# Optimization experiments

Hardware: AMD Instinct MI355X
Metric: run time of the kernel (lower is better)

The kernel has to match this reference:

```python
import jax, jax.numpy as jnp
import numpy as np

STOCH_LENGTH = 8  # default `length` in Stochify.forward


def setup_inputs() -> dict:
    key = jax.random.key(0)
    k1, k2 = jax.random.split(key)
    B, K, N = 4096, 2048, 2048
    x = jax.random.normal(k1, (B, K), dtype=jnp.float32)
    # weight init: normal(0, sqrt(2/(in+out))), shape [out, in]
    weight = jax.random.normal(k2, (N, K), dtype=jnp.float32) * np.sqrt(2.0 / (K + N))
    bias = jnp.zeros((N,), dtype=jnp.float32)
    return {"x": x, "weight": weight, "bias": bias}


def _to_stoch(key, v, length):
    """Bipolar stochastic bitstream encode: bit_l ~ Bernoulli((v+1)/2), shape [L, *v.shape]."""
    p = jnp.clip((v + 1.0) * 0.5, 0.0, 1.0)
    u = jax.random.uniform(key, (length,) + v.shape, dtype=v.dtype)
    return (u < p).astype(v.dtype)


def reference(x, weight, bias):
    # Stochify.forward: api = to_stoch(input, L); apw = to_stoch(weight.t(), L)
    # out = stoch.mm(api, apw, bipolar=True, output_stoch=False) + bias
    # Bipolar stochastic multiply is XNOR of bits; decoded product value per (i,j,k):
    #   2/L * sum_l XNOR(a,b) - 1.  Summed over k:
    #   out[i,j] = (2/L) * sum_{k,l} (2 a b - a - b + 1) - K
    # which reduces to per-slice matmuls plus row/col bit-count corrections
    # (avoids materializing the [B,K,N,L] XNOR tensor).
    L = STOCH_LENGTH
    K = x.shape[1]
    kA, kB = jax.random.split(jax.random.key(42))
    A = _to_stoch(kA, x, L)            # [L, B, K] bits in {0,1}
    Wb = _to_stoch(kB, weight.T, L)    # [L, K, N]
    S = jnp.einsum('lbk,lkn->bn', A, Wb)  # sum_{k,l} a*b
    sA = A.sum(axis=(0, 2))            # [B]  sum_{k,l} a
    sB = Wb.sum(axis=(0, 1))           # [N]  sum_{k,l} b
    xnor_count = 2.0 * S - sA[:, None] - sB[None, :] + K * L
    out = (2.0 / L) * xnor_count - K
    return out + bias[None, :]
```

## Files before the change

### kernel.cpp

```cpp
#include <hip/hip_runtime.h>
#include <stdint.h>


#define B_DIM 4096
#define K_DIM 2048
#define N_DIM 2048
#define WORDS 256

typedef unsigned long long u64;

__host__ __device__ static inline void tf2x32(uint32_t ks0, uint32_t ks1,
                                              uint32_t x0, uint32_t x1,
                                              uint32_t* o0, uint32_t* o1) {
  uint32_t ks2 = ks0 ^ ks1 ^ 0x1BD11BDAu;
  x0 += ks0; x1 += ks1;
#define TF_RND(r) { x0 += x1; x1 = (x1 << (r)) | (x1 >> (32 - (r))); x1 ^= x0; }
  TF_RND(13) TF_RND(15) TF_RND(26) TF_RND(6)
  x0 += ks1; x1 += ks2 + 1u;
  TF_RND(17) TF_RND(29) TF_RND(16) TF_RND(24)
  x0 += ks2; x1 += ks0 + 2u;
  TF_RND(13) TF_RND(15) TF_RND(26) TF_RND(6)
  x0 += ks0; x1 += ks1 + 3u;
  TF_RND(17) TF_RND(29) TF_RND(16) TF_RND(24)
  x0 += ks1; x1 += ks2 + 4u;
  TF_RND(13) TF_RND(15) TF_RND(26) TF_RND(6)
  x0 += ks2; x1 += ks0 + 5u;
  *o0 = x0; *o1 = x1;
#undef TF_RND
}

__global__ __launch_bounds__(256) void stoch_bits(const float* __restrict__ x,
                                                  const float* __restrict__ wgt,
                                                  u64* __restrict__ Ap,
                                                  u64* __restrict__ Wp,
                                                  uint32_t xk0, uint32_t xk1,
                                                  uint32_t wk0, uint32_t wk1) {
  const unsigned blk = blockIdx.x;
  const bool isW = blk >= (unsigned)B_DIM;
  const unsigned row = isW ? (blk - (unsigned)B_DIM) : blk;
  const float* src = (isW ? wgt : x) + (size_t)row * K_DIM;
  u64* dst = (isW ? Wp : Ap) + (size_t)row * WORDS;
  const uint32_t k0 = isW ? wk0 : xk0;
  const uint32_t k1 = isW ? wk1 : xk1;
  const unsigned lane = threadIdx.x & 63u;
  const unsigned wv = threadIdx.x >> 6;
#pragma unroll 1
  for (int i = 0; i < 8; ++i) {
    const unsigned kw = wv * 8u + (unsigned)i;
    const unsigned k = (kw << 6) + lane;
    const float v = src[k];
    const float p = fminf(fmaxf((v + 1.0f) * 0.5f, 0.0f), 1.0f);
    const float t = p * 8388608.0f;
    const uint32_t base = isW ? (k * 2048u + row) : (row * 2048u + k);
    u64 wbuf[8];
#pragma unroll
    for (int l = 0; l < 8; ++l) {
      uint32_t idx = base + (isW ? ((uint32_t)l << 22) : ((uint32_t)l << 23));
      uint32_t o0, o1;
      tf2x32(k0, k1, 0u, idx, &o0, &o1);
      uint32_t m = (o0 ^ o1) >> 9;
      wbuf[l] = __ballot((float)m < t);
    }
    if (lane == 0) {
#pragma unroll
      for (int l = 0; l < 8; ++l) dst[(l << 5) + kw] = wbuf[l];
    }
  }
}

__global__ __launch_bounds__(256, 4) void xnor_gemm(const u64* __restrict__ Ap,
                                                    const u64* __restrict__ Wp,
                                                    const float* __restrict__ bias,
                                                    float* __restrict__ out) {
  __shared__ u64 As[128][18];
  __shared__ u64 Ws[64][18];
  const int tid = threadIdx.x;
  const int brow = blockIdx.y << 7;
  const int bcol = blockIdx.x << 6;
  const int tx = tid & 15, ty = tid >> 4;
  uint32_t cnt[8][4] = {};
#pragma unroll 1
  for (int c = 0; c < 16; ++c) {
    if (c) __syncthreads();
#pragma unroll
    for (int i = 0; i < 4; ++i) {
      int q = tid + (i << 8);
      int r = q >> 3, c4 = q & 7;
      *(uint4*)&As[r][c4 << 1] =
          *(const uint4*)&Ap[(size_t)(brow + r) * WORDS + (c << 4) + (c4 << 1)];
    }
#pragma unroll
    for (int i = 0; i < 2; ++i) {
      int q = tid + (i << 8);
      int r = q >> 3, c4 = q & 7;
      *(uint4*)&Ws[r][c4 << 1] =
          *(const uint4*)&Wp[(size_t)(bcol + r) * WORDS + (c << 4) + (c4 << 1)];
    }
    __syncthreads();
#pragma unroll 2
    for (int wp = 0; wp < 8; ++wp) {
      uint4 av[8], bv[4];
#pragma unroll
      for (int i = 0; i < 8; ++i)
        av[i] = *(const uint4*)&As[ty + (i << 4)][wp << 1];
#pragma unroll
      for (int j = 0; j < 4; ++j)
        bv[j] = *(const uint4*)&Ws[tx + (j << 4)][wp << 1];
#pragma unroll
      for (int i = 0; i < 8; ++i)
#pragma unroll
        for (int j = 0; j < 4; ++j) {
          uint32_t t0 = av[i].x ^ bv[j].x;
          uint32_t t1 = av[i].y ^ bv[j].y;
          uint32_t t2 = av[i].z ^ bv[j].z;
          uint32_t t3 = av[i].w ^ bv[j].w;
          asm("v_bcnt_u32_b32 %0, %1, %0" : "+v"(cnt[i][j]) : "v"(t0));
          asm("v_bcnt_u32_b32 %0, %1, %0" : "+v"(cnt[i][j]) : "v"(t1));
          asm("v_bcnt_u32_b32 %0, %1, %0" : "+v"(cnt[i][j]) : "v"(t2));
          asm("v_bcnt_u32_b32 %0, %1, %0" : "+v"(cnt[i][j]) : "v"(t3));
        }
    }
  }
#pragma unroll
  for (int i = 0; i < 8; ++i) {
    int r = brow + ty + (i << 4);
#pragma unroll
    for (int j = 0; j < 4; ++j) {
      int n = bcol + tx + (j << 4);
      out[(size_t)r * N_DIM + n] = 2048.0f - 0.25f * (float)cnt[i][j] + bias[n];
    }
  }
}

extern "C" void kernel_launch(void* const* d_in, const int* in_sizes, int n_in,
                              void* d_out, int out_size, void* d_ws, size_t ws_size,
                              hipStream_t stream) {
  const float* x = (const float*)d_in[0];
  const float* wgt = (const float*)d_in[1];
  const float* bias = (const float*)d_in[2];
  float* out = (float*)d_out;

  u64* Ap = (u64*)d_ws;
  u64* Wp = Ap + (size_t)B_DIM * WORDS;

  uint32_t kA0, kA1, kB0, kB1;
  tf2x32(0u, 42u, 0u, 0u, &kA0, &kA1);
  tf2x32(0u, 42u, 0u, 1u, &kB0, &kB1);

  stoch_bits<<<B_DIM + N_DIM, 256, 0, stream>>>(x, wgt, Ap, Wp, kA0, kA1, kB0, kB1);
  dim3 grid(N_DIM / 64, B_DIM / 128);
  xnor_gemm<<<grid, 256, 0, stream>>>(Ap, Wp, bias, out);
  (void)in_sizes; (void)n_in; (void)out_size; (void)ws_size;
}
```

Measured before the change: 501.6 us.

## Replace bit-packed XNOR popcount GEMM with int8 MFMA GEMM over byte bitstreams

The encoder now writes each stochastic bit as one byte in a [row, L*K] layout and computes per-row bit counts. The XNOR-popcount kernel is replaced by an int8 MFMA GEMM (32x32x32) that loads tiles with global_load_lds and applies the row and column count corrections in the epilogue. The aim is to run the inner product on matrix cores instead of the VALU popcount path, at the cost of 8x more workspace and memory traffic. This path is taken only when the workspace is large enough, otherwise it falls back to the old kernels.

```diff
diff --git a/kernel.cpp b/kernel.cpp
--- a/kernel.cpp
+++ b/kernel.cpp
@@ -6,8 +6,11 @@
 #define K_DIM 2048
 #define N_DIM 2048
 #define WORDS 256
+#define KL 16384
 
 typedef unsigned long long u64;
+typedef int v4i __attribute__((ext_vector_type(4)));
+typedef int v16i __attribute__((ext_vector_type(16)));
 
 __host__ __device__ static inline void tf2x32(uint32_t ks0, uint32_t ks1,
                                               uint32_t x0, uint32_t x1,
@@ -29,6 +32,127 @@
 #undef TF_RND
 }
 
+
+__global__ __launch_bounds__(256) void stoch_bytes(const float* __restrict__ x,
+                                                   const float* __restrict__ wgt,
+                                                   unsigned char* __restrict__ A8,
+                                                   unsigned char* __restrict__ W8,
+                                                   float* __restrict__ sA,
+                                                   float* __restrict__ sB,
+                                                   uint32_t xk0, uint32_t xk1,
+                                                   uint32_t wk0, uint32_t wk1) {
+  __shared__ unsigned int red[4];
+  const unsigned blk = blockIdx.x;
+  const bool isW = blk >= (unsigned)B_DIM;
+  const unsigned row = isW ? (blk - (unsigned)B_DIM) : blk;
+  const float* src = (isW ? wgt : x) + (size_t)row * K_DIM;
+  unsigned char* dst = (isW ? W8 : A8) + (size_t)row * KL;
+  const uint32_t k0 = isW ? wk0 : xk0;
+  const uint32_t k1 = isW ? wk1 : xk1;
+  const unsigned lane = threadIdx.x & 63u;
+  const unsigned wv = threadIdx.x >> 6;
+  unsigned int rs = 0;
+#pragma unroll 1
+  for (int i = 0; i < 8; ++i) {
+    const unsigned kw = wv * 8u + (unsigned)i;
+    const unsigned k = (kw << 6) + lane;
+    const float v = src[k];
+    const float p = fminf(fmaxf((v + 1.0f) * 0.5f, 0.0f), 1.0f);
+    const float t = p * 8388608.0f;
+    const uint32_t base = isW ? (k * 2048u + row) : (row * 2048u + k);
+#pragma unroll
+    for (int l = 0; l < 8; ++l) {
+      uint32_t idx = base + (isW ? ((uint32_t)l << 22) : ((uint32_t)l << 23));
+      uint32_t o0, o1;
+      tf2x32(k0, k1, 0u, idx, &o0, &o1);
+      uint32_t m = (o0 ^ o1) >> 9;
+      bool bit = (float)m < t;
+      dst[(unsigned)l * 2048u + k] = bit ? 1 : 0;
+      u64 msk = __ballot(bit);
+      rs += (unsigned)__popcll(msk);
+    }
+  }
+  if (lane == 0) red[wv] = rs;
+  __syncthreads();
+  if (threadIdx.x == 0) {
+    float tot = (float)(red[0] + red[1] + red[2] + red[3]);
+    (isW ? sB : sA)[row] = tot;
+  }
+}
+
+__device__ __forceinline__ void gload16(const void* g, void* l) {
+  __builtin_amdgcn_global_load_lds((const __attribute__((address_space(1))) void*)g,
+                                   (__attribute__((address_space(3))) void*)l, 16, 0, 0);
+}
+
+__global__ __launch_bounds__(256) void i8_gemm(const unsigned char* __restrict__ A8,
+                                               const unsigned char* __restrict__ W8,
+                                               const float* __restrict__ sA,
+                                               const float* __restrict__ sB,
+                                               const float* __restrict__ bias,
+                                               float* __restrict__ out) {
+  __shared__ unsigned char As[8192];
+  __shared__ unsigned char Bs[8192];
+  const int tid = threadIdx.x;
+  const int l = tid & 63, wv = tid >> 6;
+  const int wr = wv >> 1, wc = wv & 1;
+  const int lr = l & 31, lh = l >> 5;
+  int wg = (int)blockIdx.x;
+  wg = (wg & 7) * 64 + (wg >> 3);
+  const int bx = wg & 15, by = wg >> 4;
+  const int brow = by << 7, bcol = bx << 7;
+
+  const unsigned char* pA[2];
+  const unsigned char* pB[2];
+#pragma unroll
+  for (int i = 0; i < 2; ++i) {
+    int gb = i * 4 + wv, r = gb >> 1, s = gb & 1;
+    pA[i] = A8 + (size_t)(brow + r * 32 + lr) * KL + s * 32 + lh * 16;
+    pB[i] = W8 + (size_t)(bcol + r * 32 + lr) * KL + s * 32 + lh * 16;
+  }
+  v16i acc[2][2] = {};
+#pragma unroll 1
+  for (int c = 0; c < 256; ++c) {
+    if (c) __syncthreads();
+    gload16(pA[0], As + wv * 1024);
+    gload16(pA[1], As + 4096 + wv * 1024);
+    gload16(pB[0], Bs + wv * 1024);
+    gload16(pB[1], Bs + 4096 + wv * 1024);
+    __syncthreads();
+    v4i af[2][2], bf[2][2];
+#pragma unroll
+    for (int i = 0; i < 2; ++i)
+#pragma unroll
+      for (int s = 0; s < 2; ++s) {
+        af[i][s] = *(const v4i*)(As + (((wr * 2 + i) * 2 + s) << 10) + l * 16);
+        bf[i][s] = *(const v4i*)(Bs + (((wc * 2 + i) * 2 + s) << 10) + l * 16);
+      }
+#pragma unroll
+    for (int s = 0; s < 2; ++s)
+#pragma unroll
+      for (int i = 0; i < 2; ++i)
+#pragma unroll
+        for (int j = 0; j < 2; ++j)
+          acc[i][j] = __builtin_amdgcn_mfma_i32_32x32x32_i8(af[i][s], bf[j][s],
+                                                            acc[i][j], 0, 0, 0);
+    pA[0] += 64; pA[1] += 64; pB[0] += 64; pB[1] += 64;
+  }
+#pragma unroll
+  for (int i = 0; i < 2; ++i)
+#pragma unroll
+    for (int j = 0; j < 2; ++j) {
+      const int colb = bcol + wc * 64 + j * 32 + lr;
+#pragma unroll
+      for (int reg = 0; reg < 16; ++reg) {
+        int rowb = brow + wr * 64 + i * 32 + (reg & 3) + ((reg >> 2) << 3) + (lh << 2);
+        float S = (float)acc[i][j][reg];
+        float val = (2048.0f + 0.5f * S - 0.25f * (sA[rowb] + sB[colb])) + bias[colb];
+        out[(size_t)rowb * N_DIM + colb] = val;
+      }
+    }
+}
+
+
 __global__ __launch_bounds__(256) void stoch_bits(const float* __restrict__ x,
                                                   const float* __restrict__ wgt,
                                                   u64* __restrict__ Ap,
@@ -140,15 +264,28 @@
   const float* bias = (const float*)d_in[2];
   float* out = (float*)d_out;
 
-  u64* Ap = (u64*)d_ws;
-  u64* Wp = Ap + (size_t)B_DIM * WORDS;
-
   uint32_t kA0, kA1, kB0, kB1;
   tf2x32(0u, 42u, 0u, 0u, &kA0, &kA1);
   tf2x32(0u, 42u, 0u, 1u, &kB0, &kB1);
 
-  stoch_bits<<<B_DIM + N_DIM, 256, 0, stream>>>(x, wgt, Ap, Wp, kA0, kA1, kB0, kB1);
-  dim3 grid(N_DIM / 64, B_DIM / 128);
-  xnor_gemm<<<grid, 256, 0, stream>>>(Ap, Wp, bias, out);
-  (void)in_sizes; (void)n_in; (void)out_size; (void)ws_size;
-}
+  const size_t szA8 = (size_t)B_DIM * KL;
+  const size_t szW8 = (size_t)N_DIM * KL;
+  const size_t need = szA8 + szW8 + (B_DIM + N_DIM) * sizeof(float);
+
+  if (ws_size >= need) {
+    unsigned char* A8 = (unsigned char*)d_ws;
+    unsigned char* W8 = A8 + szA8;
+    float* sA = (float*)(W8 + szW8);
+    float* sB = sA + B_DIM;
+    stoch_bytes<<<B_DIM + N_DIM, 256, 0, stream>>>(x, wgt, A8, W8, sA, sB,
+                                                   kA0, kA1, kB0, kB1);
+    i8_gemm<<<512, 256, 0, stream>>>(A8, W8, sA, sB, bias, out);
+  } else {
+    u64* Ap = (u64*)d_ws;
+    u64* Wp = Ap + (size_t)B_DIM * WORDS;
+    stoch_bits<<<B_DIM + N_DIM, 256, 0, stream>>>(x, wgt, Ap, Wp, kA0, kA1, kB0, kB1);
+    dim3 grid(N_DIM / 64, B_DIM / 128);
+    xnor_gemm<<<grid, 256, 0, stream>>>(Ap, Wp, bias, out);
+  }
+  (void)in_sizes; (void)n_in; (void)out_size;
+}
```

Measured after the change: 498.7 us. Within noise of the previous version (-0.6%).
